# Optimization experiments

Hardware: AMD Instinct MI355X
Metric: run time of the kernel (lower is better)

The kernel has to match this reference:

```python
import jax, jax.numpy as jnp
import numpy as np

N, IN_DIM, HEADS, OUT_DIM = 4096, 256, 4, 64

def setup_inputs() -> dict:
    key = jax.random.key(0)
    k1, k2, k3 = jax.random.split(key, 3)
    h = jax.random.normal(k1, (N, IN_DIM), dtype=jnp.float32)
    W = jax.random.normal(k2, (IN_DIM, HEADS * OUT_DIM), dtype=jnp.float32) * (1.0 / np.sqrt(IN_DIM))
    a = jax.random.normal(k3, (HEADS, 2 * OUT_DIM), dtype=jnp.float32) * 0.1
    return {"h": h, "W": W, "a": a}

def reference(h, W, a):
    # Wh: [N, heads, out_dim]
    Wh = (h @ W).reshape(N, HEADS, OUT_DIM)
    # Split additive attention vector a = [a_dst | a_src]; e[i,j,k] = lrelu(f_i[i,k] + f_j[j,k])
    # This is algebraically identical to LeakyReLU(((Wh_i||Wh_j) * a).sum(-1))
    f_i = jnp.einsum('nhd,hd->nh', Wh, a[:, :OUT_DIM])   # [N, heads]
    f_j = jnp.einsum('nhd,hd->nh', Wh, a[:, OUT_DIM:])   # [N, heads]
    e = jax.nn.leaky_relu(f_i[:, None, :] + f_j[None, :, :], negative_slope=0.2)  # [N,N,heads]
    attn = jax.nn.softmax(e, axis=1)  # softmax over source nodes j
    # dropout is identity in eval mode
    out = jnp.einsum('ijk,jkl->ikl', attn, Wh)  # [N, heads, out_dim]
    out = out.reshape(N, HEADS * OUT_DIM)       # concat=True
    return out, attn
```

## Files before the change

### kernel.cpp

```cpp
#include <hip/hip_runtime.h>
#include <math.h>

#define NN 4096
#define IN_DIM 256
#define HEADS 4
#define OUT_DIM 64

__device__ __forceinline__ float fexp(float x){ return __expf(x); }

__global__ void k_gw(const float* __restrict__ h, const float* __restrict__ W,
                     const float* __restrict__ a,
                     float* __restrict__ Wh, float* __restrict__ fi, float* __restrict__ fj,
                     float* __restrict__ E1j, float* __restrict__ E2j){
    __shared__ float hs[IN_DIM][17];
    const int i0 = blockIdx.x * 16;
    const int t  = threadIdx.x;
    const int hh = t >> 6, d = t & 63;
    #pragma unroll
    for (int r = 0; r < 16; ++r) hs[t][r] = h[(i0 + r) * IN_DIM + t];
    __syncthreads();
    float acc[16];
    #pragma unroll
    for (int r = 0; r < 16; ++r) acc[r] = 0.f;
    for (int k = 0; k < IN_DIM; ++k) {
        float w = W[k * 256 + t];
        #pragma unroll
        for (int r = 0; r < 16; ++r) acc[r] += hs[k][r] * w;
    }
    const float aD = a[hh * 128 + d];
    const float aS = a[hh * 128 + 64 + d];
    #pragma unroll
    for (int r = 0; r < 16; ++r) {
        Wh[(i0 + r) * 256 + t] = acc[r];
        float p1 = acc[r] * aD, p2 = acc[r] * aS;
        #pragma unroll
        for (int off = 32; off; off >>= 1) {
            p1 += __shfl_down(p1, off);
            p2 += __shfl_down(p2, off);
        }
        if (d == 0) {
            const int n = i0 + r;
            fi[n * 4 + hh]  = p1;
            fj[n * 4 + hh]  = p2;
            E1j[n * 4 + hh] = fexp(p2);
            E2j[n * 4 + hh] = fexp(0.2f * p2);
        }
    }
}

__global__ void k_rp(const float* __restrict__ fj, const float* __restrict__ Wh,
                     float* __restrict__ fs, float* __restrict__ Whp){
    const int j0 = blockIdx.x * 8;
    const int t = threadIdx.x;
    const int hh = t >> 6, d = t & 63;
    float v[8]; int cnt[8];
    #pragma unroll
    for (int r = 0; r < 8; ++r) { v[r] = fj[(j0 + r) * 4 + hh]; cnt[r] = 0; }
    for (int m = 0; m < 64; ++m) {
        const int jp = d + m * 64;
        const float x = fj[jp * 4 + hh];
        #pragma unroll
        for (int r = 0; r < 8; ++r)
            cnt[r] += (x < v[r] || (x == v[r] && jp < (j0 + r))) ? 1 : 0;
    }
    #pragma unroll
    for (int r = 0; r < 8; ++r) {
        int c = cnt[r];
        #pragma unroll
        for (int off = 32; off; off >>= 1) c += __shfl_down(c, off);
        const int rank = __shfl(c, 0);
        if (d == 0) fs[hh * NN + rank] = v[r];
        Whp[(hh * NN + rank) * 64 + d] = Wh[(j0 + r) * 256 + hh * 64 + d];
    }
}

__global__ void k_chunks(const float* __restrict__ fs, const float* __restrict__ Whp,
                         float* __restrict__ r1, float* __restrict__ r2x,
                         float* __restrict__ rz1, float* __restrict__ rz2x,
                         float* __restrict__ cs1, float* __restrict__ cs2,
                         float* __restrict__ cz1, float* __restrict__ cz2){
    const int b = blockIdx.x;
    const int H = b >> 6, c = b & 63;
    const int d = threadIdx.x;
    const int base = H * NN, q0 = c * 64;
    float a2 = 0.f, z2 = 0.f;
    #pragma unroll 4
    for (int q = q0; q < q0 + 64; ++q) {
        const float f  = fs[base + q];
        const float e2 = fexp(0.2f * f);
        const float wv = Whp[(base + q) * 64 + d];
        r2x[(base + q) * 64 + d] = a2;
        if (d == 0) rz2x[base + q] = z2;
        a2 += e2 * wv; z2 += e2;
    }
    float a1 = 0.f, z1 = 0.f;
    #pragma unroll 4
    for (int q = q0 + 63; q >= q0; --q) {
        const float f  = fs[base + q];
        const float e1 = fexp(f);
        const float wv = Whp[(base + q) * 64 + d];
        a1 += e1 * wv; z1 += e1;
        r1[(base + q) * 64 + d] = a1;
        if (d == 0) rz1[base + q] = z1;
    }
    cs1[b * 64 + d] = a1;
    cs2[b * 64 + d] = a2;
    if (d == 0) { cz1[b] = z1; cz2[b] = z2; }
}

__global__ void k_scan(const float* __restrict__ cs1, const float* __restrict__ cs2,
                       const float* __restrict__ cz1, const float* __restrict__ cz2,
                       float* __restrict__ S1, float* __restrict__ S2,
                       float* __restrict__ Z1, float* __restrict__ Z2){
    const int H = blockIdx.x;
    const int t = threadIdx.x;
    if (t < 64) {
        const int d = t; float acc = 0.f;
        S1[(H * 65 + 64) * 64 + d] = 0.f;
        #pragma unroll 8
        for (int c = 63; c >= 0; --c) { acc += cs1[(H * 64 + c) * 64 + d]; S1[(H * 65 + c) * 64 + d] = acc; }
    } else if (t < 128) {
        const int d = t - 64; float acc = 0.f;
        S2[(H * 65 + 0) * 64 + d] = 0.f;
        #pragma unroll 8
        for (int c = 0; c < 64; ++c) { acc += cs2[(H * 64 + c) * 64 + d]; S2[(H * 65 + c + 1) * 64 + d] = acc; }
    } else if (t == 128) {
        float acc = 0.f; Z1[H * 65 + 64] = 0.f;
        for (int c = 63; c >= 0; --c) { acc += cz1[H * 64 + c]; Z1[H * 65 + c] = acc; }
    } else if (t == 129) {
        float acc = 0.f; Z2[H * 65 + 0] = 0.f;
        for (int c = 0; c < 64; ++c) { acc += cz2[H * 64 + c]; Z2[H * 65 + c + 1] = acc; }
    }
}

__global__ void k_q(const float* __restrict__ fi, const float* __restrict__ fs,
                    const float* __restrict__ r1, const float* __restrict__ r2x,
                    const float* __restrict__ rz1, const float* __restrict__ rz2x,
                    const float* __restrict__ S1, const float* __restrict__ S2,
                    const float* __restrict__ Z1, const float* __restrict__ Z2,
                    float* __restrict__ out, float* __restrict__ thrE,
                    float* __restrict__ A1, float* __restrict__ A2){
    const int i = blockIdx.x;
    const int t = threadIdx.x;
    const int hh = t >> 6, d = t & 63;
    const int base = hh * NN;
    const float s = fi[i * 4 + hh];
    const float thr = -s;
    const unsigned long long m1 = __ballot(fs[base + d * 64] < thr);
    const int k1 = __popcll(m1);
    int p = 0;
    if (k1 > 0) {
        const int cc = k1 - 1;
        const unsigned long long m2 = __ballot(fs[base + cc * 64 + d] < thr);
        p = cc * 64 + __popcll(m2);
    }
    float a1, a2, z1, z2;
    if (p == NN) {
        a1 = 0.f; z1 = 0.f;
        a2 = S2[(hh * 65 + 64) * 64 + d]; z2 = Z2[hh * 65 + 64];
    } else {
        const int c = p >> 6;
        a1 = r1 [(base + p) * 64 + d] + S1[(hh * 65 + c + 1) * 64 + d];
        z1 = rz1[base + p]            + Z1[hh * 65 + c + 1];
        a2 = r2x[(base + p) * 64 + d] + S2[(hh * 65 + c) * 64 + d];
        z2 = rz2x[base + p]           + Z2[hh * 65 + c];
    }
    const float E1 = fexp(s), E2 = fexp(0.2f * s);
    const float iz = 1.f / (E1 * z1 + E2 * z2);
    out[i * 256 + t] = (E1 * a1 + E2 * a2) * iz;
    if (d == 0) {
        thrE[i * 4 + hh] = fexp(thr);
        A1[i * 4 + hh]   = E1 * iz;
        A2[i * 4 + hh]   = E2 * iz;
    }
}

__global__ void k_attn(const float4* __restrict__ E1j4, const float4* __restrict__ E2j4,
                       const float4* __restrict__ thrE4, const float4* __restrict__ A14,
                       const float4* __restrict__ A24, float4* __restrict__ attn){
    const int i = blockIdx.x;
    const float4 th = thrE4[i];
    const float4 a1 = A14[i];
    const float4 a2 = A24[i];
    float4* __restrict__ row = attn + (size_t)i * NN;
    const int t = threadIdx.x;
    #pragma unroll
    for (int it = 0; it < 16; ++it) {
        const int j = it * 256 + t;
        const float4 e1 = E1j4[j];
        const float4 e2 = E2j4[j];
        float4 o;
        o.x = (e1.x >= th.x) ? a1.x * e1.x : a2.x * e2.x;
        o.y = (e1.y >= th.y) ? a1.y * e1.y : a2.y * e2.y;
        o.z = (e1.z >= th.z) ? a1.z * e1.z : a2.z * e2.z;
        o.w = (e1.w >= th.w) ? a1.w * e1.w : a2.w * e2.w;
        row[j] = o;
    }
}

extern "C" void kernel_launch(void* const* d_in, const int* in_sizes, int n_in,
                              void* d_out, int out_size, void* d_ws, size_t ws_size,
                              hipStream_t stream) {
    const float* h = (const float*)d_in[0];
    const float* W = (const float*)d_in[1];
    const float* a = (const float*)d_in[2];
    float* out = (float*)d_out;
    float* ws  = (float*)d_ws;

    float* Wh   = ws;
    float* Whp  = Wh   + 1048576;
    float* fi   = Whp  + 1048576;
    float* fj   = fi   + 16384;
    float* E1j  = fj   + 16384;
    float* E2j  = E1j  + 16384;
    float* fs   = E2j  + 16384;
    float* cs1  = fs   + 16384;
    float* cs2  = cs1  + 16384;
    float* cz1  = cs2  + 16384;
    float* cz2  = cz1  + 256;
    float* S1   = cz2  + 256;
    float* S2   = S1   + 16640;
    float* Z1   = S2   + 16640;
    float* Z2   = Z1   + 260;
    float* r1   = Z2   + 260;
    float* r2x  = r1   + 1048576;
    float* rz1  = r2x  + 1048576;
    float* rz2x = rz1  + 16384;
    float* thrE = rz2x + 16384;
    float* A1   = thrE + 16384;
    float* A2   = A1   + 16384;

    k_gw    <<<NN / 16, 256, 0, stream>>>(h, W, a, Wh, fi, fj, E1j, E2j);
    k_rp    <<<NN / 8, 256, 0, stream>>>(fj, Wh, fs, Whp);
    k_chunks<<<HEADS * 64, 64, 0, stream>>>(fs, Whp, r1, r2x, rz1, rz2x, cs1, cs2, cz1, cz2);
    k_scan  <<<HEADS, 256, 0, stream>>>(cs1, cs2, cz1, cz2, S1, S2, Z1, Z2);
    k_q     <<<NN, 256, 0, stream>>>(fi, fs, r1, r2x, rz1, rz2x, S1, S2, Z1, Z2, out, thrE, A1, A2);

    float* attn = out + (NN * HEADS * OUT_DIM);
    k_attn  <<<NN, 256, 0, stream>>>((const float4*)E1j, (const float4*)E2j,
                                     (const float4*)thrE, (const float4*)A1,
                                     (const float4*)A2, (float4*)attn);
}
```

Measured before the change: 158.2 us.

## Parallelize chunk scan across four warps and drop LDS staging in projection GEMM

The chunk prefix-sum kernel now uses 256 threads per block. Each of four wavefronts scans a 16-element sub-chunk in registers, then the sub-chunks are combined through shared memory offsets. This replaces a serial 64-step loop run by a single wavefront. Separately, the projection kernel reads h directly from global memory, relying on broadcast and cache, instead of staging it in LDS. That removes a sync but risks more load traffic.

```diff
diff --git a/kernel.cpp b/kernel.cpp
--- a/kernel.cpp
+++ b/kernel.cpp
@@ -12,20 +12,18 @@
                      const float* __restrict__ a,
                      float* __restrict__ Wh, float* __restrict__ fi, float* __restrict__ fj,
                      float* __restrict__ E1j, float* __restrict__ E2j){
-    __shared__ float hs[IN_DIM][17];
     const int i0 = blockIdx.x * 16;
     const int t  = threadIdx.x;
     const int hh = t >> 6, d = t & 63;
-    #pragma unroll
-    for (int r = 0; r < 16; ++r) hs[t][r] = h[(i0 + r) * IN_DIM + t];
-    __syncthreads();
     float acc[16];
     #pragma unroll
     for (int r = 0; r < 16; ++r) acc[r] = 0.f;
+    #pragma unroll 4
     for (int k = 0; k < IN_DIM; ++k) {
-        float w = W[k * 256 + t];
-        #pragma unroll
-        for (int r = 0; r < 16; ++r) acc[r] += hs[k][r] * w;
+        const float w = W[k * 256 + t];
+        #pragma unroll
+        for (int r = 0; r < 16; ++r)
+            acc[r] += h[(i0 + r) * IN_DIM + k] * w;
     }
     const float aD = a[hh * 128 + d];
     const float aS = a[hh * 128 + 64 + d];
@@ -81,31 +79,60 @@
                          float* __restrict__ cz1, float* __restrict__ cz2){
     const int b = blockIdx.x;
     const int H = b >> 6, c = b & 63;
-    const int d = threadIdx.x;
-    const int base = H * NN, q0 = c * 64;
-    float a2 = 0.f, z2 = 0.f;
-    #pragma unroll 4
-    for (int q = q0; q < q0 + 64; ++q) {
-        const float f  = fs[base + q];
-        const float e2 = fexp(0.2f * f);
-        const float wv = Whp[(base + q) * 64 + d];
-        r2x[(base + q) * 64 + d] = a2;
-        if (d == 0) rz2x[base + q] = z2;
-        a2 += e2 * wv; z2 += e2;
-    }
-    float a1 = 0.f, z1 = 0.f;
-    #pragma unroll 4
-    for (int q = q0 + 63; q >= q0; --q) {
-        const float f  = fs[base + q];
-        const float e1 = fexp(f);
-        const float wv = Whp[(base + q) * 64 + d];
-        a1 += e1 * wv; z1 += e1;
-        r1[(base + q) * 64 + d] = a1;
-        if (d == 0) rz1[base + q] = z1;
-    }
-    cs1[b * 64 + d] = a1;
-    cs2[b * 64 + d] = a2;
-    if (d == 0) { cz1[b] = z1; cz2[b] = z2; }
+    const int t = threadIdx.x;
+    const int w = t >> 6, d = t & 63;
+    const int base = H * NN;
+    const int qw = c * 64 + w * 16;
+    float wv[16], e1s[16], e2s[16];
+    #pragma unroll
+    for (int s = 0; s < 16; ++s) {
+        const int q = qw + s;
+        const float f = fs[base + q];
+        e1s[s] = fexp(f);
+        e2s[s] = fexp(0.2f * f);
+        wv[s]  = Whp[(size_t)(base + q) * 64 + d];
+    }
+    float p2[16], s1[16], lz1[16], lz2[16];
+    float acc2 = 0.f, z2 = 0.f;
+    #pragma unroll
+    for (int s = 0; s < 16; ++s) {
+        p2[s] = acc2; lz2[s] = z2;
+        acc2 += e2s[s] * wv[s]; z2 += e2s[s];
+    }
+    float acc1 = 0.f, z1 = 0.f;
+    #pragma unroll
+    for (int s = 15; s >= 0; --s) {
+        acc1 += e1s[s] * wv[s]; z1 += e1s[s];
+        s1[s] = acc1; lz1[s] = z1;
+    }
+    __shared__ float t1[4][64], t2[4][64], tz1[4], tz2[4];
+    t1[w][d] = acc1; t2[w][d] = acc2;
+    if (d == 0) { tz1[w] = z1; tz2[w] = z2; }
+    __syncthreads();
+    float off1 = 0.f, off2 = 0.f, zo1 = 0.f, zo2 = 0.f;
+    #pragma unroll
+    for (int w2 = 0; w2 < 4; ++w2) {
+        if (w2 > w) { off1 += t1[w2][d]; zo1 += tz1[w2]; }
+        if (w2 < w) { off2 += t2[w2][d]; zo2 += tz2[w2]; }
+    }
+    #pragma unroll
+    for (int s = 0; s < 16; ++s) {
+        const int q = qw + s;
+        r1 [(size_t)(base + q) * 64 + d] = off1 + s1[s];
+        r2x[(size_t)(base + q) * 64 + d] = off2 + p2[s];
+        if (d == 0) {
+            rz1 [base + q] = zo1 + lz1[s];
+            rz2x[base + q] = zo2 + lz2[s];
+        }
+    }
+    if (w == 0) {
+        cs1[b * 64 + d] = off1 + acc1;
+        if (d == 0) cz1[b] = zo1 + z1;
+    }
+    if (w == 3) {
+        cs2[b * 64 + d] = off2 + acc2;
+        if (d == 0) cz2[b] = zo2 + z2;
+    }
 }
 
 __global__ void k_scan(const float* __restrict__ cs1, const float* __restrict__ cs2,
@@ -232,7 +259,7 @@
 
     k_gw    <<<NN / 16, 256, 0, stream>>>(h, W, a, Wh, fi, fj, E1j, E2j);
     k_rp    <<<NN / 8, 256, 0, stream>>>(fj, Wh, fs, Whp);
-    k_chunks<<<HEADS * 64, 64, 0, stream>>>(fs, Whp, r1, r2x, rz1, rz2x, cs1, cs2, cz1, cz2);
+    k_chunks<<<HEADS * 64, 256, 0, stream>>>(fs, Whp, r1, r2x, rz1, rz2x, cs1, cs2, cz1, cz2);
     k_scan  <<<HEADS, 256, 0, stream>>>(cs1, cs2, cz1, cz2, S1, S2, Z1, Z2);
     k_q     <<<NN, 256, 0, stream>>>(fi, fs, r1, r2x, rz1, rz2x, S1, S2, Z1, Z2, out, thrE, A1, A2);
 
```

Measured after the change: 149.1 us. 1.06x faster.
